# Kernel tuning notes

Measured on AMD Instinct MI355X. Metric: run time of the kernel, lower is better.

## Reference

```python
import jax, jax.numpy as jnp
import numpy as np

B, N, E = 16, 4096, 65536
IN, H = 256, 512
G1, G2 = 32, 32
M1, M2 = 1024, 32768
GOD = 8
BN_EPS = 1e-5


def setup_inputs() -> dict:
    key = jax.random.key(0)
    ks = jax.random.split(key, 16)
    rn = lambda i, sh, s=0.05: jax.random.normal(ks[i], sh, dtype=jnp.float32) * s
    return {
        "x": jax.random.normal(ks[0], (B, IN), dtype=jnp.float32),
        "smoothed_vert_pos": jax.random.normal(ks[1], (B, N * 3), dtype=jnp.float32),
        "hidden": jnp.zeros((B, H), jnp.float32),
        "edge_index": jax.random.randint(ks[2], (2, E), 0, N),
        "W0": rn(3, (G1, 3), 0.3), "a0_src": rn(4, (G1,), 0.3), "a0_dst": rn(5, (G1,), 0.3), "b0": jnp.zeros((G1,), jnp.float32),
        "W1": rn(6, (G2, G1), 0.2), "a1_src": rn(7, (G2,), 0.2), "a1_dst": rn(8, (G2,), 0.2), "b1": jnp.zeros((G2,), jnp.float32),
        "w_ih": rn(9, (3 * H, IN)), "w_hh": rn(10, (3 * H, H)),
        "b_ih": jnp.zeros((3 * H,), jnp.float32), "b_hh": jnp.zeros((3 * H,), jnp.float32),
        "lin1_w": rn(11, (M1, H)), "lin1_b": jnp.zeros((M1,), jnp.float32),
        "prelu1": jnp.full((M1,), 0.25, jnp.float32), "bn1_g": jnp.ones((M1,), jnp.float32), "bn1_b": jnp.zeros((M1,), jnp.float32),
        "lin2_w": rn(12, (M2, M1), 0.02), "lin2_b": jnp.zeros((M2,), jnp.float32),
        "prelu2": jnp.full((M2,), 0.25, jnp.float32), "bn2_g": jnp.ones((M2,), jnp.float32), "bn2_b": jnp.zeros((M2,), jnp.float32),
        "w_out": rn(13, (3, G2 + GOD), 0.2), "b_out": jnp.zeros((3,), jnp.float32),
    }


def _gat(v, src, dst, W, a_s, a_d, b):
    # PyG GATConv, heads=1, eval mode (no dropout), self-loops already in src/dst
    h = v @ W.T                                           # [N, F]
    e = jax.nn.leaky_relu((h * a_s).sum(-1)[src] + (h * a_d).sum(-1)[dst], 0.2)  # [E+N]
    m = jax.ops.segment_max(e, dst, num_segments=N)       # segment-softmax over incoming edges
    w = jnp.exp(e - m[dst])
    s = jax.ops.segment_sum(w, dst, num_segments=N)
    coef = w / s[dst]
    return jax.ops.segment_sum(coef[:, None] * h[src], dst, num_segments=N) + b


def _mlp_layer(t, w, bb, p, g, be):
    t = t @ w.T + bb                                      # Linear
    t = jnp.where(t >= 0, t, p * t)                       # PReLU (per-channel)
    # eval BatchNorm1d with running_mean=0, running_var=1
    return (t / jnp.sqrt(1.0 + BN_EPS)) * g + be


def reference(x, smoothed_vert_pos, hidden, edge_index,
              W0, a0_src, a0_dst, b0, W1, a1_src, a1_dst, b1,
              w_ih, w_hh, b_ih, b_hh,
              lin1_w, lin1_b, prelu1, bn1_g, bn1_b,
              lin2_w, lin2_b, prelu2, bn2_g, bn2_b,
              w_out, b_out):
    sv = smoothed_vert_pos.reshape(B, N, 3)
    loop = jnp.arange(N, dtype=edge_index.dtype)
    src = jnp.concatenate([edge_index[0], loop])          # GATConv add_self_loops=True
    dst = jnp.concatenate([edge_index[1], loop])
    gat0 = jax.vmap(lambda v: _gat(v, src, dst, W0, a0_src, a0_dst, b0))(sv)   # [B,N,G1]
    gat1 = jax.vmap(lambda v: _gat(v, src, dst, W1, a1_src, a1_dst, b1))(gat0)  # [B,N,G2]

    # GRUCell
    gi = x @ w_ih.T + b_ih
    gh = hidden @ w_hh.T + b_hh
    ir, iz, inn = jnp.split(gi, 3, axis=-1)
    hr, hz, hn = jnp.split(gh, 3, axis=-1)
    r = jax.nn.sigmoid(ir + hr)
    z = jax.nn.sigmoid(iz + hz)
    n = jnp.tanh(inn + r * hn)
    next_hidden = (1.0 - z) * n + z * hidden              # [B,H]

    o = _mlp_layer(next_hidden, lin1_w, lin1_b, prelu1, bn1_g, bn1_b)
    o = _mlp_layer(o, lin2_w, lin2_b, prelu2, bn2_g, bn2_b)
    gru_out = o.reshape(B, N, GOD)

    y = (jnp.concatenate([gru_out, gat1], axis=2) @ w_out.T + b_out).reshape(B, -1)
    return y, next_hidden
```

## Files before the change

### kernel.cpp

```cpp
#include <hip/hip_runtime.h>

#define BB 16
#define NN 4096
#define EE 65536
#define HH 512
#define M1N 1024
#define M2N 32768
#define CAP 96

typedef unsigned short ushortT;
typedef short   s8v   __attribute__((ext_vector_type(8)));
typedef float   f4v   __attribute__((ext_vector_type(4)));

__device__ inline ushortT f2b(float x) {
  unsigned u = __float_as_uint(x);
  return (ushortT)((u + 0x7FFFu + ((u >> 16) & 1u)) >> 16);
}



__global__ void k_pre(int* __restrict__ cnt,
                      const float* __restrict__ x, const float* __restrict__ hid,
                      const float* __restrict__ w_ih, const float* __restrict__ w_hh,
                      const float* __restrict__ b_ih, const float* __restrict__ b_hh,
                      float* __restrict__ nh, float* __restrict__ out_nh,
                      const float* __restrict__ svp, const float* __restrict__ W0,
                      const float* __restrict__ a0s, const float* __restrict__ a0d,
                      float* __restrict__ h0t, float* __restrict__ as0t,
                      float* __restrict__ ad0t) {
  const int bid = blockIdx.x;
  if (bid < 16) {
    cnt[bid * 256 + threadIdx.x] = 0;
    return;
  }
  if (bid < 2064) {
    int wid = (bid - 16) * 4 + (threadIdx.x >> 6);
    int lane = threadIdx.x & 63;
    int b = wid >> 9, j = wid & 511;
    const float* xb = x + b * 256;
    const float* hb = hid + b * HH;
    float ir = 0.f, iz = 0.f, in_ = 0.f, hr = 0.f, hz = 0.f, hn = 0.f;
    for (int k = lane; k < 256; k += 64) {
      float xv = xb[k];
      ir  += xv * w_ih[(size_t)j * 256 + k];
      iz  += xv * w_ih[(size_t)(j + 512) * 256 + k];
      in_ += xv * w_ih[(size_t)(j + 1024) * 256 + k];
    }
    for (int k = lane; k < 512; k += 64) {
      float hv = hb[k];
      hr += hv * w_hh[(size_t)j * 512 + k];
      hz += hv * w_hh[(size_t)(j + 512) * 512 + k];
      hn += hv * w_hh[(size_t)(j + 1024) * 512 + k];
    }
#pragma unroll
    for (int m = 1; m < 64; m <<= 1) {
      ir += __shfl_xor(ir, m, 64); iz += __shfl_xor(iz, m, 64); in_ += __shfl_xor(in_, m, 64);
      hr += __shfl_xor(hr, m, 64); hz += __shfl_xor(hz, m, 64); hn  += __shfl_xor(hn, m, 64);
    }
    if (lane == 0) {
      ir += b_ih[j]; iz += b_ih[j + 512]; in_ += b_ih[j + 1024];
      hr += b_hh[j]; hz += b_hh[j + 512]; hn += b_hh[j + 1024];
      float r = 1.f / (1.f + __expf(-(ir + hr)));
      float z = 1.f / (1.f + __expf(-(iz + hz)));
      float n = tanhf(in_ + r * hn);
      float v = (1.f - z) * n + z * hb[j];
      nh[wid] = v;
      out_nh[wid] = v;
    }
    return;
  }
  int gid = (bid - 2064) * 256 + threadIdx.x;
  int grp = gid >> 5, f = gid & 31;
  int b = grp >> 12, n = grp & 4095;
  const float* v = svp + (size_t)grp * 3;
  float hv = v[0] * W0[f * 3] + v[1] * W0[f * 3 + 1] + v[2] * W0[f * 3 + 2];
  h0t[(size_t)n * 512 + b * 32 + f] = hv;
  float ps = hv * a0s[f], pd = hv * a0d[f];
#pragma unroll
  for (int m = 1; m < 32; m <<= 1) {
    ps += __shfl_xor(ps, m, 64);
    pd += __shfl_xor(pd, m, 64);
  }
  if (f == 0) { as0t[n * 16 + b] = ps; ad0t[n * 16 + b] = pd; }
}


__global__ void k_fill2(const int* __restrict__ src, const int* __restrict__ dst,
                        int* __restrict__ cnt, int* __restrict__ csr) {
  int k = blockIdx.x * 256 + threadIdx.x;
  if (k < EE) {
    int d = dst[k];
    int slot = atomicAdd(&cnt[d], 1);
    if ((unsigned)slot < CAP) csr[d * CAP + slot] = src[k];
  }
}


__global__ void k_mid(const int* __restrict__ cnt, const int* __restrict__ csr,
                      const float* __restrict__ h0t, const float* __restrict__ as0t,
                      const float* __restrict__ ad0t, const float* __restrict__ b0,
                      const float* __restrict__ W1, const float* __restrict__ a1s,
                      const float* __restrict__ a1d,
                      float* __restrict__ h1t, float* __restrict__ as1t,
                      float* __restrict__ ad1t,
                      const float* __restrict__ nh, const float* __restrict__ l1w,
                      const float* __restrict__ l1b, const float* __restrict__ p1,
                      const float* __restrict__ g1v, const float* __restrict__ be1,
                      ushortT* __restrict__ o1b) {
  const int bid = blockIdx.x;
  const int wave = threadIdx.x >> 6;
  const int lane = threadIdx.x & 63;
  if (bid < 2048) {
    __shared__ float lds[4][8][36];
    const int n  = bid * 2 + (wave >> 1);
    const int bh = wave & 1;
    const int bl = lane >> 3;
    const int fq = lane & 7;
    const int b  = bh * 8 + bl;
    const int f0 = fq * 4;
    const int boff = b * 32 + f0;
    const int deg = min(cnt[n], CAP);
    const int base = n * CAP;
    const float adn = ad0t[n * 16 + b];
    const int total = deg + 1;
    float4 acc = {0.f, 0.f, 0.f, 0.f};
    float asum = 0.f;
    for (int i = 0; i < total; i += 4) {
      int r0 = csr[base + i];
      int r1 = csr[base + i + 1];
      int r2 = csr[base + i + 2];
      int r3 = csr[base + i + 3];
      int sv0 = (i     < deg) ? r0 : n;
      int sv1 = (i + 1 < deg) ? r1 : n;
      int sv2 = (i + 2 < deg) ? r2 : n;
      int sv3 = (i + 3 < deg) ? r3 : n;
      float e0 = as0t[sv0 * 16 + b];
      float e1 = as0t[sv1 * 16 + b];
      float e2 = as0t[sv2 * 16 + b];
      float e3 = as0t[sv3 * 16 + b];
      float4 hv0 = *(const float4*)(h0t + (size_t)sv0 * 512 + boff);
      float4 hv1 = *(const float4*)(h0t + (size_t)sv1 * 512 + boff);
      float4 hv2 = *(const float4*)(h0t + (size_t)sv2 * 512 + boff);
      float4 hv3 = *(const float4*)(h0t + (size_t)sv3 * 512 + boff);
      float e, w;
      e = e0 + adn; e = e >= 0.f ? e : 0.2f * e;
      w = (i     < total) ? __expf(e) : 0.f;
      asum += w; acc.x += w*hv0.x; acc.y += w*hv0.y; acc.z += w*hv0.z; acc.w += w*hv0.w;
      e = e1 + adn; e = e >= 0.f ? e : 0.2f * e;
      w = (i + 1 < total) ? __expf(e) : 0.f;
      asum += w; acc.x += w*hv1.x; acc.y += w*hv1.y; acc.z += w*hv1.z; acc.w += w*hv1.w;
      e = e2 + adn; e = e >= 0.f ? e : 0.2f * e;
      w = (i + 2 < total) ? __expf(e) : 0.f;
      asum += w; acc.x += w*hv2.x; acc.y += w*hv2.y; acc.z += w*hv2.z; acc.w += w*hv2.w;
      e = e3 + adn; e = e >= 0.f ? e : 0.2f * e;
      w = (i + 3 < total) ? __expf(e) : 0.f;
      asum += w; acc.x += w*hv3.x; acc.y += w*hv3.y; acc.z += w*hv3.z; acc.w += w*hv3.w;
    }
    float inv = 1.f / asum;
    float4 b0v = *(const float4*)(b0 + f0);
    float4 g0;
    g0.x = acc.x * inv + b0v.x; g0.y = acc.y * inv + b0v.y;
    g0.z = acc.z * inv + b0v.z; g0.w = acc.w * inv + b0v.w;
    *(float4*)&lds[wave][bl][f0] = g0;
    __syncthreads();
    float h1a = 0.f, h1b = 0.f, h1c = 0.f, h1d = 0.f;
    const float* gr = lds[wave][bl];
    const float* w1r = W1 + f0 * 32;
#pragma unroll
    for (int k = 0; k < 32; ++k) {
      float gk = gr[k];
      h1a += gk * w1r[k];
      h1b += gk * w1r[32 + k];
      h1c += gk * w1r[64 + k];
      h1d += gk * w1r[96 + k];
    }
    float4 h1v = {h1a, h1b, h1c, h1d};
    *(float4*)(h1t + (size_t)n * 512 + boff) = h1v;
    float ps = h1a * a1s[f0] + h1b * a1s[f0+1] + h1c * a1s[f0+2] + h1d * a1s[f0+3];
    float pd = h1a * a1d[f0] + h1b * a1d[f0+1] + h1c * a1d[f0+2] + h1d * a1d[f0+3];
#pragma unroll
    for (int m = 1; m < 8; m <<= 1) {
      ps += __shfl_xor(ps, m, 64);
      pd += __shfl_xor(pd, m, 64);
    }
    if (fq == 0) { as1t[n * 16 + b] = ps; ad1t[n * 16 + b] = pd; }
    return;
  }
  int wid = (bid - 2048) * 4 + wave;
  int b = wid >> 10, j = wid & 1023;
  const float* hb = nh + b * HH;
  const float* wr = l1w + (size_t)j * HH;
  float acc = 0.f;
  for (int k = lane; k < HH; k += 64) acc += hb[k] * wr[k];
#pragma unroll
  for (int m = 1; m < 64; m <<= 1) acc += __shfl_xor(acc, m, 64);
  if (lane == 0) {
    float t = acc + l1b[j];
    t = t >= 0.f ? t : p1[j] * t;
    o1b[wid] = f2b(t * 0.99999500003749973f * g1v[j] + be1[j]);
  }
}


__global__ __launch_bounds__(256) void k_lin2m(
    const ushortT* __restrict__ o1b, const float* __restrict__ l2w,
    const float* __restrict__ bias, const float* __restrict__ pr,
    const float* __restrict__ g, const float* __restrict__ be,
    float* __restrict__ o2) {
  __shared__ f4v plds[4][64];
  const int wave = threadIdx.x >> 6;
  const int lane = threadIdx.x & 63;
  const int r16 = lane & 15;
  const int chunk = lane >> 4;
  const int j0 = blockIdx.x * 16;
  const int kbase = wave * 256 + chunk * 8;
  const s8v* ap = (const s8v*)(o1b + r16 * 1024 + kbase);
  const f4v* bp = (const f4v*)(l2w + (size_t)(j0 + r16) * 1024 + kbase);
  f4v acc = {0.f, 0.f, 0.f, 0.f};
#pragma unroll
  for (int it = 0; it < 8; ++it) {
    s8v a = ap[it * 4];
    f4v w0 = __builtin_nontemporal_load(bp + it * 8);
    f4v w1 = __builtin_nontemporal_load(bp + it * 8 + 1);
    s8v b;
    b[0] = (short)f2b(w0[0]); b[1] = (short)f2b(w0[1]);
    b[2] = (short)f2b(w0[2]); b[3] = (short)f2b(w0[3]);
    b[4] = (short)f2b(w1[0]); b[5] = (short)f2b(w1[1]);
    b[6] = (short)f2b(w1[2]); b[7] = (short)f2b(w1[3]);
    acc = __builtin_amdgcn_mfma_f32_16x16x32_bf16(a, b, acc, 0, 0, 0);
  }
  plds[wave][lane] = acc;
  __syncthreads();
  if (wave == 0) {
    f4v s0 = plds[0][lane];
    f4v s1 = plds[1][lane];
    f4v s2 = plds[2][lane];
    f4v s3 = plds[3][lane];
    f4v s = s0 + s1 + s2 + s3;
    const int j = j0 + r16;
    const float bj = bias[j], pj = pr[j], gj = g[j], bej = be[j];
    const float INV = 0.99999500003749973f;
#pragma unroll
    for (int r = 0; r < 4; ++r) {
      int b = chunk * 4 + r;
      float t = s[r] + bj;
      t = t >= 0.f ? t : pj * t;
      o2[(size_t)b * M2N + j] = t * INV * gj + bej;
    }
  }
}


__global__ void k_fin(const int* __restrict__ cnt, const int* __restrict__ csr,
                      const float* __restrict__ h1t, const float* __restrict__ as1t,
                      const float* __restrict__ ad1t, const float* __restrict__ b1,
                      const float* __restrict__ o2, const float* __restrict__ wout,
                      const float* __restrict__ bout, float* __restrict__ y) {
  const int wave = threadIdx.x >> 6;
  const int lane = threadIdx.x & 63;
  const int n  = blockIdx.x * 2 + (wave >> 1);
  const int bh = wave & 1;
  const int bl = lane >> 3;
  const int fq = lane & 7;
  const int b  = bh * 8 + bl;
  const int f0 = fq * 4;
  const int boff = b * 32 + f0;
  const int deg = min(cnt[n], CAP);
  const int base = n * CAP;
  const float adn = ad1t[n * 16 + b];
  const int total = deg + 1;
  float4 acc = {0.f, 0.f, 0.f, 0.f};
  float asum = 0.f;
  for (int i = 0; i < total; i += 4) {
    int r0 = csr[base + i];
    int r1 = csr[base + i + 1];
    int r2 = csr[base + i + 2];
    int r3 = csr[base + i + 3];
    int sv0 = (i     < deg) ? r0 : n;
    int sv1 = (i + 1 < deg) ? r1 : n;
    int sv2 = (i + 2 < deg) ? r2 : n;
    int sv3 = (i + 3 < deg) ? r3 : n;
    float e0 = as1t[sv0 * 16 + b];
    float e1 = as1t[sv1 * 16 + b];
    float e2 = as1t[sv2 * 16 + b];
    float e3 = as1t[sv3 * 16 + b];
    float4 hv0 = *(const float4*)(h1t + (size_t)sv0 * 512 + boff);
    float4 hv1 = *(const float4*)(h1t + (size_t)sv1 * 512 + boff);
    float4 hv2 = *(const float4*)(h1t + (size_t)sv2 * 512 + boff);
    float4 hv3 = *(const float4*)(h1t + (size_t)sv3 * 512 + boff);
    float e, w;
    e = e0 + adn; e = e >= 0.f ? e : 0.2f * e;
    w = (i     < total) ? __expf(e) : 0.f;
    asum += w; acc.x += w*hv0.x; acc.y += w*hv0.y; acc.z += w*hv0.z; acc.w += w*hv0.w;
    e = e1 + adn; e = e >= 0.f ? e : 0.2f * e;
    w = (i + 1 < total) ? __expf(e) : 0.f;
    asum += w; acc.x += w*hv1.x; acc.y += w*hv1.y; acc.z += w*hv1.z; acc.w += w*hv1.w;
    e = e2 + adn; e = e >= 0.f ? e : 0.2f * e;
    w = (i + 2 < total) ? __expf(e) : 0.f;
    asum += w; acc.x += w*hv2.x; acc.y += w*hv2.y; acc.z += w*hv2.z; acc.w += w*hv2.w;
    e = e3 + adn; e = e >= 0.f ? e : 0.2f * e;
    w = (i + 3 < total) ? __expf(e) : 0.f;
    asum += w; acc.x += w*hv3.x; acc.y += w*hv3.y; acc.z += w*hv3.z; acc.w += w*hv3.w;
  }
  float inv = 1.f / asum;
  float4 b1v = *(const float4*)(b1 + f0);
  float gx = acc.x * inv + b1v.x, gy = acc.y * inv + b1v.y;
  float gz = acc.z * inv + b1v.z, gw = acc.w * inv + b1v.w;
  float pc0 = gx*wout[ 8+f0] + gy*wout[ 9+f0] + gz*wout[10+f0] + gw*wout[11+f0];
  float pc1 = gx*wout[48+f0] + gy*wout[49+f0] + gz*wout[50+f0] + gw*wout[51+f0];
  float pc2 = gx*wout[88+f0] + gy*wout[89+f0] + gz*wout[90+f0] + gw*wout[91+f0];
#pragma unroll
  for (int m = 1; m < 8; m <<= 1) {
    pc0 += __shfl_xor(pc0, m, 64);
    pc1 += __shfl_xor(pc1, m, 64);
    pc2 += __shfl_xor(pc2, m, 64);
  }
  if (fq == 0) {
    const float* gr = o2 + (size_t)b * M2N + n * 8;
    float4 ga = *(const float4*)gr;
    float4 gb = *(const float4*)(gr + 4);
    float c0 = pc0 + bout[0], c1 = pc1 + bout[1], c2 = pc2 + bout[2];
    c0 += ga.x*wout[0]  + ga.y*wout[1]  + ga.z*wout[2]  + ga.w*wout[3]
        + gb.x*wout[4]  + gb.y*wout[5]  + gb.z*wout[6]  + gb.w*wout[7];
    c1 += ga.x*wout[40] + ga.y*wout[41] + ga.z*wout[42] + ga.w*wout[43]
        + gb.x*wout[44] + gb.y*wout[45] + gb.z*wout[46] + gb.w*wout[47];
    c2 += ga.x*wout[80] + ga.y*wout[81] + ga.z*wout[82] + ga.w*wout[83]
        + gb.x*wout[84] + gb.y*wout[85] + gb.z*wout[86] + gb.w*wout[87];
    float* yp = y + (size_t)b * (NN * 3) + n * 3;
    yp[0] = c0; yp[1] = c1; yp[2] = c2;
  }
}


extern "C" void kernel_launch(void* const* d_in, const int* in_sizes, int n_in,
                              void* d_out, int out_size, void* d_ws, size_t ws_size,
                              hipStream_t stream) {
  const float* x    = (const float*)d_in[0];
  const float* svp  = (const float*)d_in[1];
  const float* hid  = (const float*)d_in[2];
  const int*   ei   = (const int*)d_in[3];
  const float* W0   = (const float*)d_in[4];
  const float* a0s  = (const float*)d_in[5];
  const float* a0d  = (const float*)d_in[6];
  const float* b0   = (const float*)d_in[7];
  const float* W1   = (const float*)d_in[8];
  const float* a1s  = (const float*)d_in[9];
  const float* a1d  = (const float*)d_in[10];
  const float* b1   = (const float*)d_in[11];
  const float* w_ih = (const float*)d_in[12];
  const float* w_hh = (const float*)d_in[13];
  const float* b_ih = (const float*)d_in[14];
  const float* b_hh = (const float*)d_in[15];
  const float* l1w  = (const float*)d_in[16];
  const float* l1b  = (const float*)d_in[17];
  const float* p1   = (const float*)d_in[18];
  const float* g1v  = (const float*)d_in[19];
  const float* be1  = (const float*)d_in[20];
  const float* l2w  = (const float*)d_in[21];
  const float* l2b  = (const float*)d_in[22];
  const float* p2   = (const float*)d_in[23];
  const float* g2v  = (const float*)d_in[24];
  const float* be2  = (const float*)d_in[25];
  const float* wout = (const float*)d_in[26];
  const float* bout = (const float*)d_in[27];
  float* out = (float*)d_out;

  char* ws = (char*)d_ws;
  size_t off = 0;
  auto alloc = [&](size_t bytes) -> char* {
    char* p = ws + off;
    off += (bytes + 255) & ~(size_t)255;
    return p;
  };
  int*     cnt   = (int*)alloc((size_t)NN * 4);
  int*     csr   = (int*)alloc(((size_t)NN * CAP + 16) * 4);
  float*   h0t   = (float*)alloc((size_t)NN * 16 * 32 * 4);
  float*   as0t  = (float*)alloc((size_t)NN * 16 * 4);
  float*   ad0t  = (float*)alloc((size_t)NN * 16 * 4);
  float*   h1t   = (float*)alloc((size_t)NN * 16 * 32 * 4);
  float*   as1t  = (float*)alloc((size_t)NN * 16 * 4);
  float*   ad1t  = (float*)alloc((size_t)NN * 16 * 4);
  float*   nh    = (float*)alloc((size_t)BB * HH * 4);
  ushortT* o1b   = (ushortT*)alloc((size_t)BB * M1N * 2);
  float*   o2    = (float*)alloc((size_t)BB * M2N * 4);

  const int* srcv = ei;
  const int* dstv = ei + EE;

  k_pre<<<16 + 2048 + 8192, 256, 0, stream>>>(
      cnt, x, hid, w_ih, w_hh, b_ih, b_hh, nh, out + (size_t)BB * NN * 3,
      svp, W0, a0s, a0d, h0t, as0t, ad0t);
  k_fill2<<<EE / 256, 256, 0, stream>>>(srcv, dstv, cnt, csr);
  k_mid<<<2048 + 4096, 256, 0, stream>>>(
      cnt, csr, h0t, as0t, ad0t, b0, W1, a1s, a1d, h1t, as1t, ad1t,
      nh, l1w, l1b, p1, g1v, be1, o1b);
  k_lin2m<<<M2N / 16, 256, 0, stream>>>(o1b, l2w, l2b, p2, g2v, be2, o2);
  k_fin<<<2048, 256, 0, stream>>>(cnt, csr, h1t, as1t, ad1t, b1, o2, wout, bout, out);
}
```

Before: 126.0 us.

## Regroup launches: fuse lin1 with CSR fill, interleave lin2 MFMA with GAT layer

Moves the lin1 GEMV into the same launch as the CSR fill. The first GAT aggregation now shares a kernel with the bf16 MFMA lin2 GEMM, using even and odd blocks in alternation and a shared-memory union. This cuts one kernel launch. It also lets the bandwidth-heavy lin2 weight stream overlap with the latency-bound gather work on the GPU. The nontemporal loads on the lin2 weights were dropped, which may change cache behaviour for the large weight stream.

```diff
diff --git a/kernel.cpp b/kernel.cpp
--- a/kernel.cpp
+++ b/kernel.cpp
@@ -85,9 +85,32 @@
 }
 
 
-__global__ void k_fill2(const int* __restrict__ src, const int* __restrict__ dst,
-                        int* __restrict__ cnt, int* __restrict__ csr) {
-  int k = blockIdx.x * 256 + threadIdx.x;
+__global__ void k_mid1(const float* __restrict__ nh, const float* __restrict__ l1w,
+                       const float* __restrict__ l1b, const float* __restrict__ p1,
+                       const float* __restrict__ g1v, const float* __restrict__ be1,
+                       ushortT* __restrict__ o1b,
+                       const int* __restrict__ src, const int* __restrict__ dst,
+                       int* __restrict__ cnt, int* __restrict__ csr) {
+  const int bid = blockIdx.x;
+  if (bid < 4096) {
+    const int wave = threadIdx.x >> 6;
+    const int lane = threadIdx.x & 63;
+    int wid = bid * 4 + wave;
+    int b = wid >> 10, j = wid & 1023;
+    const float* hb = nh + b * HH;
+    const float* wr = l1w + (size_t)j * HH;
+    float acc = 0.f;
+    for (int k = lane; k < HH; k += 64) acc += hb[k] * wr[k];
+#pragma unroll
+    for (int m = 1; m < 64; m <<= 1) acc += __shfl_xor(acc, m, 64);
+    if (lane == 0) {
+      float t = acc + l1b[j];
+      t = t >= 0.f ? t : p1[j] * t;
+      o1b[wid] = f2b(t * 0.99999500003749973f * g1v[j] + be1[j]);
+    }
+    return;
+  }
+  int k = (bid - 4096) * 256 + threadIdx.x;
   if (k < EE) {
     int d = dst[k];
     int slot = atomicAdd(&cnt[d], 1);
@@ -96,158 +119,134 @@
 }
 
 
-__global__ void k_mid(const int* __restrict__ cnt, const int* __restrict__ csr,
-                      const float* __restrict__ h0t, const float* __restrict__ as0t,
-                      const float* __restrict__ ad0t, const float* __restrict__ b0,
-                      const float* __restrict__ W1, const float* __restrict__ a1s,
-                      const float* __restrict__ a1d,
-                      float* __restrict__ h1t, float* __restrict__ as1t,
-                      float* __restrict__ ad1t,
-                      const float* __restrict__ nh, const float* __restrict__ l1w,
-                      const float* __restrict__ l1b, const float* __restrict__ p1,
-                      const float* __restrict__ g1v, const float* __restrict__ be1,
-                      ushortT* __restrict__ o1b) {
+__global__ __launch_bounds__(256) void k_big(
+    const ushortT* __restrict__ o1b, const float* __restrict__ l2w,
+    const float* __restrict__ l2b, const float* __restrict__ p2,
+    const float* __restrict__ g2v, const float* __restrict__ be2,
+    float* __restrict__ o2,
+    const int* __restrict__ cnt, const int* __restrict__ csr,
+    const float* __restrict__ h0t, const float* __restrict__ as0t,
+    const float* __restrict__ ad0t, const float* __restrict__ b0,
+    const float* __restrict__ W1, const float* __restrict__ a1s,
+    const float* __restrict__ a1d,
+    float* __restrict__ h1t, float* __restrict__ as1t,
+    float* __restrict__ ad1t) {
   const int bid = blockIdx.x;
   const int wave = threadIdx.x >> 6;
   const int lane = threadIdx.x & 63;
-  if (bid < 2048) {
-    __shared__ float lds[4][8][36];
-    const int n  = bid * 2 + (wave >> 1);
-    const int bh = wave & 1;
-    const int bl = lane >> 3;
-    const int fq = lane & 7;
-    const int b  = bh * 8 + bl;
-    const int f0 = fq * 4;
-    const int boff = b * 32 + f0;
-    const int deg = min(cnt[n], CAP);
-    const int base = n * CAP;
-    const float adn = ad0t[n * 16 + b];
-    const int total = deg + 1;
-    float4 acc = {0.f, 0.f, 0.f, 0.f};
-    float asum = 0.f;
-    for (int i = 0; i < total; i += 4) {
-      int r0 = csr[base + i];
-      int r1 = csr[base + i + 1];
-      int r2 = csr[base + i + 2];
-      int r3 = csr[base + i + 3];
-      int sv0 = (i     < deg) ? r0 : n;
-      int sv1 = (i + 1 < deg) ? r1 : n;
-      int sv2 = (i + 2 < deg) ? r2 : n;
-      int sv3 = (i + 3 < deg) ? r3 : n;
-      float e0 = as0t[sv0 * 16 + b];
-      float e1 = as0t[sv1 * 16 + b];
-      float e2 = as0t[sv2 * 16 + b];
-      float e3 = as0t[sv3 * 16 + b];
-      float4 hv0 = *(const float4*)(h0t + (size_t)sv0 * 512 + boff);
-      float4 hv1 = *(const float4*)(h0t + (size_t)sv1 * 512 + boff);
-      float4 hv2 = *(const float4*)(h0t + (size_t)sv2 * 512 + boff);
-      float4 hv3 = *(const float4*)(h0t + (size_t)sv3 * 512 + boff);
-      float e, w;
-      e = e0 + adn; e = e >= 0.f ? e : 0.2f * e;
-      w = (i     < total) ? __expf(e) : 0.f;
-      asum += w; acc.x += w*hv0.x; acc.y += w*hv0.y; acc.z += w*hv0.z; acc.w += w*hv0.w;
-      e = e1 + adn; e = e >= 0.f ? e : 0.2f * e;
-      w = (i + 1 < total) ? __expf(e) : 0.f;
-      asum += w; acc.x += w*hv1.x; acc.y += w*hv1.y; acc.z += w*hv1.z; acc.w += w*hv1.w;
-      e = e2 + adn; e = e >= 0.f ? e : 0.2f * e;
-      w = (i + 2 < total) ? __expf(e) : 0.f;
-      asum += w; acc.x += w*hv2.x; acc.y += w*hv2.y; acc.z += w*hv2.z; acc.w += w*hv2.w;
-      e = e3 + adn; e = e >= 0.f ? e : 0.2f * e;
-      w = (i + 3 < total) ? __expf(e) : 0.f;
-      asum += w; acc.x += w*hv3.x; acc.y += w*hv3.y; acc.z += w*hv3.z; acc.w += w*hv3.w;
-    }
-    float inv = 1.f / asum;
-    float4 b0v = *(const float4*)(b0 + f0);
-    float4 g0;
-    g0.x = acc.x * inv + b0v.x; g0.y = acc.y * inv + b0v.y;
-    g0.z = acc.z * inv + b0v.z; g0.w = acc.w * inv + b0v.w;
-    *(float4*)&lds[wave][bl][f0] = g0;
+  __shared__ union {
+    f4v p[4][64];
+    float g[4][8][36];
+  } sh;
+  if ((bid & 1) == 0) {
+    const int r16 = lane & 15;
+    const int chunk = lane >> 4;
+    const int j0 = (bid >> 1) * 16;
+    const int kbase = wave * 256 + chunk * 8;
+    const s8v* ap = (const s8v*)(o1b + r16 * 1024 + kbase);
+    const f4v* bp = (const f4v*)(l2w + (size_t)(j0 + r16) * 1024 + kbase);
+    f4v acc = {0.f, 0.f, 0.f, 0.f};
+#pragma unroll
+    for (int it = 0; it < 8; ++it) {
+      s8v a = ap[it * 4];
+      f4v w0 = bp[it * 8];
+      f4v w1 = bp[it * 8 + 1];
+      s8v b;
+      b[0] = (short)f2b(w0[0]); b[1] = (short)f2b(w0[1]);
+      b[2] = (short)f2b(w0[2]); b[3] = (short)f2b(w0[3]);
+      b[4] = (short)f2b(w1[0]); b[5] = (short)f2b(w1[1]);
+      b[6] = (short)f2b(w1[2]); b[7] = (short)f2b(w1[3]);
+      acc = __builtin_amdgcn_mfma_f32_16x16x32_bf16(a, b, acc, 0, 0, 0);
+    }
+    sh.p[wave][lane] = acc;
     __syncthreads();
-    float h1a = 0.f, h1b = 0.f, h1c = 0.f, h1d = 0.f;
-    const float* gr = lds[wave][bl];
-    const float* w1r = W1 + f0 * 32;
-#pragma unroll
-    for (int k = 0; k < 32; ++k) {
-      float gk = gr[k];
-      h1a += gk * w1r[k];
-      h1b += gk * w1r[32 + k];
-      h1c += gk * w1r[64 + k];
-      h1d += gk * w1r[96 + k];
-    }
-    float4 h1v = {h1a, h1b, h1c, h1d};
-    *(float4*)(h1t + (size_t)n * 512 + boff) = h1v;
-    float ps = h1a * a1s[f0] + h1b * a1s[f0+1] + h1c * a1s[f0+2] + h1d * a1s[f0+3];
-    float pd = h1a * a1d[f0] + h1b * a1d[f0+1] + h1c * a1d[f0+2] + h1d * a1d[f0+3];
-#pragma unroll
-    for (int m = 1; m < 8; m <<= 1) {
-      ps += __shfl_xor(ps, m, 64);
-      pd += __shfl_xor(pd, m, 64);
-    }
-    if (fq == 0) { as1t[n * 16 + b] = ps; ad1t[n * 16 + b] = pd; }
+    if (wave == 0) {
+      f4v s = sh.p[0][lane] + sh.p[1][lane] + sh.p[2][lane] + sh.p[3][lane];
+      const int j = j0 + r16;
+      const float bj = l2b[j], pj = p2[j], gj = g2v[j], bej = be2[j];
+      const float INV = 0.99999500003749973f;
+#pragma unroll
+      for (int r = 0; r < 4; ++r) {
+        int b = chunk * 4 + r;
+        float t = s[r] + bj;
+        t = t >= 0.f ? t : pj * t;
+        o2[(size_t)b * M2N + j] = t * INV * gj + bej;
+      }
+    }
     return;
   }
-  int wid = (bid - 2048) * 4 + wave;
-  int b = wid >> 10, j = wid & 1023;
-  const float* hb = nh + b * HH;
-  const float* wr = l1w + (size_t)j * HH;
-  float acc = 0.f;
-  for (int k = lane; k < HH; k += 64) acc += hb[k] * wr[k];
-#pragma unroll
-  for (int m = 1; m < 64; m <<= 1) acc += __shfl_xor(acc, m, 64);
-  if (lane == 0) {
-    float t = acc + l1b[j];
-    t = t >= 0.f ? t : p1[j] * t;
-    o1b[wid] = f2b(t * 0.99999500003749973f * g1v[j] + be1[j]);
-  }
-}
-
-
-__global__ __launch_bounds__(256) void k_lin2m(
-    const ushortT* __restrict__ o1b, const float* __restrict__ l2w,
-    const float* __restrict__ bias, const float* __restrict__ pr,
-    const float* __restrict__ g, const float* __restrict__ be,
-    float* __restrict__ o2) {
-  __shared__ f4v plds[4][64];
-  const int wave = threadIdx.x >> 6;
-  const int lane = threadIdx.x & 63;
-  const int r16 = lane & 15;
-  const int chunk = lane >> 4;
-  const int j0 = blockIdx.x * 16;
-  const int kbase = wave * 256 + chunk * 8;
-  const s8v* ap = (const s8v*)(o1b + r16 * 1024 + kbase);
-  const f4v* bp = (const f4v*)(l2w + (size_t)(j0 + r16) * 1024 + kbase);
-  f4v acc = {0.f, 0.f, 0.f, 0.f};
-#pragma unroll
-  for (int it = 0; it < 8; ++it) {
-    s8v a = ap[it * 4];
-    f4v w0 = __builtin_nontemporal_load(bp + it * 8);
-    f4v w1 = __builtin_nontemporal_load(bp + it * 8 + 1);
-    s8v b;
-    b[0] = (short)f2b(w0[0]); b[1] = (short)f2b(w0[1]);
-    b[2] = (short)f2b(w0[2]); b[3] = (short)f2b(w0[3]);
-    b[4] = (short)f2b(w1[0]); b[5] = (short)f2b(w1[1]);
-    b[6] = (short)f2b(w1[2]); b[7] = (short)f2b(w1[3]);
-    acc = __builtin_amdgcn_mfma_f32_16x16x32_bf16(a, b, acc, 0, 0, 0);
-  }
-  plds[wave][lane] = acc;
+  const int n  = (bid >> 1) * 2 + (wave >> 1);
+  const int bh = wave & 1;
+  const int bl = lane >> 3;
+  const int fq = lane & 7;
+  const int b  = bh * 8 + bl;
+  const int f0 = fq * 4;
+  const int boff = b * 32 + f0;
+  const int deg = min(cnt[n], CAP);
+  const int base = n * CAP;
+  const float adn = ad0t[n * 16 + b];
+  const int total = deg + 1;
+  float4 acc = {0.f, 0.f, 0.f, 0.f};
+  float asum = 0.f;
+  for (int i = 0; i < total; i += 4) {
+    int r0 = csr[base + i];
+    int r1 = csr[base + i + 1];
+    int r2 = csr[base + i + 2];
+    int r3 = csr[base + i + 3];
+    int sv0 = (i     < deg) ? r0 : n;
+    int sv1 = (i + 1 < deg) ? r1 : n;
+    int sv2 = (i + 2 < deg) ? r2 : n;
+    int sv3 = (i + 3 < deg) ? r3 : n;
+    float e0 = as0t[sv0 * 16 + b];
+    float e1 = as0t[sv1 * 16 + b];
+    float e2 = as0t[sv2 * 16 + b];
+    float e3 = as0t[sv3 * 16 + b];
+    float4 hv0 = *(const float4*)(h0t + (size_t)sv0 * 512 + boff);
+    float4 hv1 = *(const float4*)(h0t + (size_t)sv1 * 512 + boff);
+    float4 hv2 = *(const float4*)(h0t + (size_t)sv2 * 512 + boff);
+    float4 hv3 = *(const float4*)(h0t + (size_t)sv3 * 512 + boff);
+    float e, w;
+    e = e0 + adn; e = e >= 0.f ? e : 0.2f * e;
+    w = (i     < total) ? __expf(e) : 0.f;
+    asum += w; acc.x += w*hv0.x; acc.y += w*hv0.y; acc.z += w*hv0.z; acc.w += w*hv0.w;
+    e = e1 + adn; e = e >= 0.f ? e : 0.2f * e;
+    w = (i + 1 < total) ? __expf(e) : 0.f;
+    asum += w; acc.x += w*hv1.x; acc.y += w*hv1.y; acc.z += w*hv1.z; acc.w += w*hv1.w;
+    e = e2 + adn; e = e >= 0.f ? e : 0.2f * e;
+    w = (i + 2 < total) ? __expf(e) : 0.f;
+    asum += w; acc.x += w*hv2.x; acc.y += w*hv2.y; acc.z += w*hv2.z; acc.w += w*hv2.w;
+    e = e3 + adn; e = e >= 0.f ? e : 0.2f * e;
+    w = (i + 3 < total) ? __expf(e) : 0.f;
+    asum += w; acc.x += w*hv3.x; acc.y += w*hv3.y; acc.z += w*hv3.z; acc.w += w*hv3.w;
+  }
+  float inv = 1.f / asum;
+  float4 b0v = *(const float4*)(b0 + f0);
+  float4 g0;
+  g0.x = acc.x * inv + b0v.x; g0.y = acc.y * inv + b0v.y;
+  g0.z = acc.z * inv + b0v.z; g0.w = acc.w * inv + b0v.w;
+  *(float4*)&sh.g[wave][bl][f0] = g0;
   __syncthreads();
-  if (wave == 0) {
-    f4v s0 = plds[0][lane];
-    f4v s1 = plds[1][lane];
-    f4v s2 = plds[2][lane];
-    f4v s3 = plds[3][lane];
-    f4v s = s0 + s1 + s2 + s3;
-    const int j = j0 + r16;
-    const float bj = bias[j], pj = pr[j], gj = g[j], bej = be[j];
-    const float INV = 0.99999500003749973f;
-#pragma unroll
-    for (int r = 0; r < 4; ++r) {
-      int b = chunk * 4 + r;
-      float t = s[r] + bj;
-      t = t >= 0.f ? t : pj * t;
-      o2[(size_t)b * M2N + j] = t * INV * gj + bej;
-    }
-  }
+  float h1a = 0.f, h1b = 0.f, h1c = 0.f, h1d = 0.f;
+  const float* gr = sh.g[wave][bl];
+  const float* w1r = W1 + f0 * 32;
+#pragma unroll
+  for (int k = 0; k < 32; ++k) {
+    float gk = gr[k];
+    h1a += gk * w1r[k];
+    h1b += gk * w1r[32 + k];
+    h1c += gk * w1r[64 + k];
+    h1d += gk * w1r[96 + k];
+  }
+  float4 h1v = {h1a, h1b, h1c, h1d};
+  *(float4*)(h1t + (size_t)n * 512 + boff) = h1v;
+  float ps = h1a * a1s[f0] + h1b * a1s[f0+1] + h1c * a1s[f0+2] + h1d * a1s[f0+3];
+  float pd = h1a * a1d[f0] + h1b * a1d[f0+1] + h1c * a1d[f0+2] + h1d * a1d[f0+3];
+#pragma unroll
+  for (int m = 1; m < 8; m <<= 1) {
+    ps += __shfl_xor(ps, m, 64);
+    pd += __shfl_xor(pd, m, 64);
+  }
+  if (fq == 0) { as1t[n * 16 + b] = ps; ad1t[n * 16 + b] = pd; }
 }
 
 
@@ -390,10 +389,10 @@
   k_pre<<<16 + 2048 + 8192, 256, 0, stream>>>(
       cnt, x, hid, w_ih, w_hh, b_ih, b_hh, nh, out + (size_t)BB * NN * 3,
       svp, W0, a0s, a0d, h0t, as0t, ad0t);
-  k_fill2<<<EE / 256, 256, 0, stream>>>(srcv, dstv, cnt, csr);
-  k_mid<<<2048 + 4096, 256, 0, stream>>>(
-      cnt, csr, h0t, as0t, ad0t, b0, W1, a1s, a1d, h1t, as1t, ad1t,
-      nh, l1w, l1b, p1, g1v, be1, o1b);
-  k_lin2m<<<M2N / 16, 256, 0, stream>>>(o1b, l2w, l2b, p2, g2v, be2, o2);
+  k_mid1<<<4096 + 256, 256, 0, stream>>>(
+      nh, l1w, l1b, p1, g1v, be1, o1b, srcv, dstv, cnt, csr);
+  k_big<<<4096, 256, 0, stream>>>(
+      o1b, l2w, l2b, p2, g2v, be2, o2,
+      cnt, csr, h0t, as0t, ad0t, b0, W1, a1s, a1d, h1t, as1t, ad1t);
   k_fin<<<2048, 256, 0, stream>>>(cnt, csr, h1t, as1t, ad1t, b1, o2, wout, bout, out);
 }
```

New measurement: 140.2 us. 11.3% more time.
